# Optimization experiments

Measured on AMD Instinct MI355X. Metric: run time of the kernel, lower is better.

## Reference

```python
import jax, jax.numpy as jnp
import numpy as np

N, F, H, D = 50000, 128, 8, 16   # nodes, node features, heads, per-head dim (F == H*D -> Identity residual)
E, G = 800000, 512               # edges, graphs
HD = H * D


def _xavier(key, shape):
    fan = sum(shape[-2:]) if len(shape) >= 2 else shape[0] + 1
    lim = (6.0 / (shape[-2] + shape[-1])) ** 0.5 if len(shape) >= 2 else (6.0 / fan) ** 0.5
    return jax.random.uniform(key, shape, jnp.float32, -lim, lim)


def setup_inputs() -> dict:
    key = jax.random.key(0)
    ks = jax.random.split(key, 10)
    x = jax.random.normal(ks[0], (N, F), jnp.float32)
    edge_index = jax.random.randint(ks[1], (2, E), 0, N, dtype=jnp.int64)
    batch = jnp.sort(jax.random.randint(ks[2], (N,), 0, G, dtype=jnp.int64))
    W_src = _xavier(ks[3], (HD, F))
    W_dst = _xavier(ks[4], (HD, F))
    double_attn = _xavier(ks[5], (1, H, D))  # xavier over last two dims
    bias = jnp.zeros((HD,), jnp.float32)
    prelu_alpha = jnp.float32(0.25)          # nn.PReLU() default single weight
    w_weighting = _xavier(ks[6], (1, HD))
    b_weighting = jnp.zeros((1,), jnp.float32)
    w_score = _xavier(ks[7], (HD, HD))
    b_score = jnp.zeros((HD,), jnp.float32)
    return {
        "x": x, "edge_index": edge_index, "batch": batch,
        "W_src": W_src, "W_dst": W_dst, "double_attn": double_attn,
        "bias": bias, "prelu_alpha": prelu_alpha,
        "w_weighting": w_weighting, "b_weighting": b_weighting,
        "w_score": w_score, "b_score": b_score,
    }


def reference(x, edge_index, batch, W_src, W_dst, double_attn, bias, prelu_alpha,
              w_weighting, b_weighting, w_score, b_score):
    src, dst = edge_index[0], edge_index[1]
    # dropout is identity in eval mode
    src_p = (x @ W_src.T).reshape(N, H, D)    # [N,H,D]
    dst_p = (x @ W_dst.T).reshape(N, H, D)
    # edge-wise attention logits: gather + LeakyReLU(0.2) + dot with attention vector
    e = src_p[src] + dst_p[dst]               # [E,H,D]
    e = jnp.where(e > 0, e, 0.2 * e)
    logits = jnp.einsum('ehd,ohd->eh', e, double_attn)  # [E,H] (double_attn has leading 1)
    # segment softmax over destination nodes (global max shift, as in original)
    exp = jnp.exp(logits - logits.max())
    denom = jax.ops.segment_sum(exp, dst, num_segments=N)  # [N,H]
    alpha = exp / (denom[dst] + 1e-16)        # [E,H]
    # weighted aggregation of source projections
    msg = src_p[src] * alpha[:, :, None]      # [E,H,D]
    out = jax.ops.segment_sum(msg, dst, num_segments=N)    # [N,H,D]
    out = out + x.reshape(N, H, D)            # residual (Identity since F == H*D)
    out = out.reshape(N, HD) + bias           # concat heads + bias
    out = jnp.where(out > 0, out, prelu_alpha * out)       # PReLU activation
    # ReadoutPhase: gated sum pooling + max pooling per graph, concatenated
    weighted = jax.nn.sigmoid(out @ w_weighting.T + b_weighting)  # [N,1]
    score = out @ w_score.T + b_score                              # [N,HD]
    g_sum = jax.ops.segment_sum(weighted * score, batch, num_segments=G)  # [G,HD]
    g_max = jax.ops.segment_max(out, batch, num_segments=G)              # [G,HD]
    readout = jnp.concatenate([g_sum, g_max], axis=1)                     # [G,2*HD]
    return out, readout
```

## Files before the change

### kernel.cpp

```cpp
#include <hip/hip_runtime.h>

#define NODES 50000
#define FEAT 128
#define EDGES 800000
#define GRAPHS 512
#define NB 196
#define CHUNK 4096
#define ABLK 196
#define BCAP 8192
#define PROJ_BLOCKS 782

typedef unsigned int u32;
typedef unsigned short u16;
typedef __attribute__((ext_vector_type(8))) short short8;
typedef __attribute__((ext_vector_type(4))) float v4f;
typedef __attribute__((ext_vector_type(4))) u32 u32x4;
typedef __attribute__((ext_vector_type(2))) float f2;

static __device__ __forceinline__ float bflo(u32 u){ return __uint_as_float(u << 16); }
static __device__ __forceinline__ float bfhi(u32 u){ return __uint_as_float(u & 0xffff0000u); }
static __device__ __forceinline__ u16 f2bf(float f){
  u32 u = __float_as_uint(f);
  u32 r = u + 0x7fffu + ((u >> 16) & 1u);
  return (u16)(r >> 16);
}
static __device__ __forceinline__ u32 packbf(float a, float b){
  return (u32)f2bf(a) | ((u32)f2bf(b) << 16);
}
static __device__ __forceinline__ f2 unpk(u32 u){ f2 r; r.x = bflo(u); r.y = bfhi(u); return r; }
static __device__ __forceinline__ f2 vmax2(f2 a, f2 b){ f2 r; r.x = fmaxf(a.x,b.x); r.y = fmaxf(a.y,b.y); return r; }

#define LROW 68
__global__ __launch_bounds__(256) void proj_hist_kernel(
    const float* __restrict__ x, const float* __restrict__ Wsrc,
    const float* __restrict__ Wdst, u16* __restrict__ srcp, u16* __restrict__ dstp,
    const int* __restrict__ ei, int* __restrict__ bcount)
{
  __shared__ u32 x_lds[64 * LROW];
  __shared__ int cnt[NB];
  const int t = threadIdx.x;

  if (blockIdx.x >= PROJ_BLOCKS){
    const int b = blockIdx.x - PROJ_BLOCKS;
    for (int k = t; k < NB; k += 256) cnt[k] = 0;
    __syncthreads();
    const int e0 = b * CHUNK;
    const int e1 = (e0 + CHUNK < EDGES) ? e0 + CHUNK : EDGES;
    for (int e = e0 + t; e < e1; e += 256)
      atomicAdd(&cnt[ei[EDGES + e] >> 8], 1);
    __syncthreads();
    for (int k = t; k < NB; k += 256) bcount[b * NB + k] = cnt[k];
    return;
  }

  const int node0 = blockIdx.x * 64;
  const int rows_valid = NODES - node0 < 64 ? NODES - node0 : 64;
  const float4* xp = (const float4*)(x + (size_t)node0 * 128);
  for (int idx = t; idx < rows_valid * 32; idx += 256){
    const float4 v = xp[idx];
    const int row = idx >> 5, cq = idx & 31;
    x_lds[row * LROW + cq * 2]     = packbf(v.x, v.y);
    x_lds[row * LROW + cq * 2 + 1] = packbf(v.z, v.w);
  }

  const int wave = t >> 6, lane = t & 63;
  const int r16 = lane & 15;
  const int quad = lane >> 4;
  const int ko = quad * 4;
  const int n0 = wave * 32;

  short8 bs[2][4], bd[2][4];
  #pragma unroll
  for (int nt = 0; nt < 2; ++nt){
    const int col = n0 + nt * 16 + r16;
    #pragma unroll
    for (int k = 0; k < 4; ++k){
      const float4* wp = (const float4*)(Wsrc + col * 128 + quad * 8 + k * 32);
      float4 w0 = wp[0], w1 = wp[1];
      u32x4 pk; pk.x = packbf(w0.x,w0.y); pk.y = packbf(w0.z,w0.w);
      pk.z = packbf(w1.x,w1.y); pk.w = packbf(w1.z,w1.w);
      bs[nt][k] = __builtin_bit_cast(short8, pk);
      const float4* vp = (const float4*)(Wdst + col * 128 + quad * 8 + k * 32);
      float4 v0 = vp[0], v1 = vp[1];
      u32x4 qk; qk.x = packbf(v0.x,v0.y); qk.y = packbf(v0.z,v0.w);
      qk.z = packbf(v1.x,v1.y); qk.w = packbf(v1.z,v1.w);
      bd[nt][k] = __builtin_bit_cast(short8, qk);
    }
  }
  __syncthreads();

  #pragma unroll
  for (int mt = 0; mt < 4; ++mt){
    const int node_base = node0 + mt * 16;
    if (node_base >= NODES) break;
    short8 afr[4];
    #pragma unroll
    for (int k = 0; k < 4; ++k)
      afr[k] = *(const short8*)&x_lds[(mt * 16 + r16) * LROW + ko + k * 16];
    v4f s0 = {0.f,0.f,0.f,0.f}, s1 = s0, d0 = s0, d1 = s0;
    #pragma unroll
    for (int k = 0; k < 4; ++k){
      s0 = __builtin_amdgcn_mfma_f32_16x16x32_bf16(afr[k], bs[0][k], s0, 0, 0, 0);
      s1 = __builtin_amdgcn_mfma_f32_16x16x32_bf16(afr[k], bs[1][k], s1, 0, 0, 0);
      d0 = __builtin_amdgcn_mfma_f32_16x16x32_bf16(afr[k], bd[0][k], d0, 0, 0, 0);
      d1 = __builtin_amdgcn_mfma_f32_16x16x32_bf16(afr[k], bd[1][k], d1, 0, 0, 0);
    }
    const int node = node_base + quad * 4;
    u16* so0 = srcp + ((size_t)(wave*2)   * NODES + node) * 16 + r16;
    u16* so1 = srcp + ((size_t)(wave*2+1) * NODES + node) * 16 + r16;
    u16* dd0 = dstp + ((size_t)(wave*2)   * NODES + node) * 16 + r16;
    u16* dd1 = dstp + ((size_t)(wave*2+1) * NODES + node) * 16 + r16;
    #pragma unroll
    for (int r = 0; r < 4; ++r){
      so0[r * 16] = f2bf(s0[r]);
      so1[r * 16] = f2bf(s1[r]);
      dd0[r * 16] = f2bf(d0[r]);
      dd1[r * 16] = f2bf(d1[r]);
    }
  }
}

__global__ __launch_bounds__(256) void bucket_scatter_kernel(
    const int* __restrict__ ei, const int* __restrict__ bcount,
    int* __restrict__ bstart_g, u32* __restrict__ ebuf, float* __restrict__ wsum)
{
  __shared__ int tot[256];
  __shared__ int bstart_s[NB + 1];
  __shared__ int obase_s[NB];
  __shared__ int cur[NB];
  const int b = blockIdx.x, t = threadIdx.x;
  const int nid = b * 256 + t;
  if (nid < NODES) wsum[nid] = 0.f;
  int total = 0, obase = 0;
  if (t < NB){
    int run = 0;
    for (int q = 0; q < ABLK; ++q){
      if (q == b) obase = run;
      run += bcount[q * NB + t];
    }
    total = run;
  }
  tot[t] = total;
  __syncthreads();
  const int v = total;
  for (int off = 1; off < 256; off <<= 1){
    const int add = (t >= off) ? tot[t - off] : 0;
    __syncthreads();
    tot[t] += add;
    __syncthreads();
  }
  if (t < NB){
    bstart_s[t] = tot[t] - v;
    obase_s[t] = obase;
    cur[t] = 0;
  }
  if (t == NB - 1) bstart_s[NB] = tot[t];
  __syncthreads();
  if (b == 0 && t <= NB) bstart_g[t] = bstart_s[t];

  const int e0 = b * CHUNK;
  const int e1 = (e0 + CHUNK < EDGES) ? e0 + CHUNK : EDGES;
  for (int e = e0 + t; e < e1; e += 256){
    const int d = ei[EDGES + e];
    const int s = ei[e];
    const int k = d >> 8;
    const int r = atomicAdd(&cur[k], 1);
    ebuf[bstart_s[k] + obase_s[k] + r] = (u32)s | ((u32)(d & 255) << 16);
  }
}

__global__ __launch_bounds__(256) void bucket_csr_kernel(
    const u32* __restrict__ ebuf, const int* __restrict__ bstart,
    int* __restrict__ row_start, u16* __restrict__ srclist)
{
  __shared__ int cnt[256], excl[256], cur[256];
  __shared__ u32 loc[BCAP];
  const int k = blockIdx.x, t = threadIdx.x;
  const int base = bstart[k];
  int ne = bstart[k + 1] - base;
  if (ne > BCAP) ne = BCAP;
  cnt[t] = 0;
  __syncthreads();
  for (int j = t; j < ne; j += 256)
    atomicAdd(&cnt[(ebuf[base + j] >> 16) & 255], 1);
  __syncthreads();
  const int v = cnt[t];
  for (int off = 1; off < 256; off <<= 1){
    const int add = (t >= off) ? cnt[t - off] : 0;
    __syncthreads();
    cnt[t] += add;
    __syncthreads();
  }
  excl[t] = cnt[t] - v;
  cur[t] = cnt[t] - v;
  __syncthreads();
  const int node = k * 256 + t;
  if (node <= NODES) row_start[node] = base + excl[t];
  for (int j = t; j < ne; j += 256){
    const u32 e = ebuf[base + j];
    const int p = atomicAdd(&cur[(e >> 16) & 255], 1);
    loc[p] = e & 0xFFFFu;
  }
  __syncthreads();
  for (int j = t; j < ne; j += 256)
    srclist[base + j] = (u16)loc[j];
}

__global__ __launch_bounds__(256, 4) void aggregate_kernel(
    const u16* __restrict__ srcp, const u16* __restrict__ dstp,
    const int* __restrict__ row_start, const u16* __restrict__ srclist,
    const float* __restrict__ x, const float* __restrict__ attn,
    const float* __restrict__ bias, const float* __restrict__ palpha,
    const float* __restrict__ ww, float* __restrict__ outp,
    float* __restrict__ wsum)
{
  const int h   = blockIdx.x & 7;
  const int grp = blockIdx.x >> 3;
  const int wv = threadIdx.x >> 6;
  const int lane = threadIdx.x & 63;
  const int nd = lane >> 3;
  const int es = lane & 7;
  const int i = grp * 32 + wv * 8 + nd;
  const bool vn = i < NODES;
  const int ic = vn ? i : NODES - 1;
  const size_t hN = (size_t)h * NODES;
  const uint4* sp = (const uint4*)srcp;

  f2 d2[8], a2[8];
  {
    const uint4 dA = ((const uint4*)dstp)[(hN + ic) * 2];
    const uint4 dB = ((const uint4*)dstp)[(hN + ic) * 2 + 1];
    d2[0]=unpk(dA.x); d2[1]=unpk(dA.y); d2[2]=unpk(dA.z); d2[3]=unpk(dA.w);
    d2[4]=unpk(dB.x); d2[5]=unpk(dB.y); d2[6]=unpk(dB.z); d2[7]=unpk(dB.w);
    const float4* ap = (const float4*)(attn + h * 16);
    const float4 a0 = ap[0], a1 = ap[1], a2v = ap[2], a3v = ap[3];
    a2[0].x=a0.x;  a2[0].y=a0.y;  a2[1].x=a0.z;  a2[1].y=a0.w;
    a2[2].x=a1.x;  a2[2].y=a1.y;  a2[3].x=a1.z;  a2[3].y=a1.w;
    a2[4].x=a2v.x; a2[4].y=a2v.y; a2[5].x=a2v.z; a2[5].y=a2v.w;
    a2[6].x=a3v.x; a2[6].y=a3v.y; a2[7].x=a3v.z; a2[7].y=a3v.w;
  }
  const int lo = vn ? row_start[i] : 0;
  const int hi = vn ? row_start[i + 1] : 0;
  const int deg = hi - lo;
  const int nb = (deg + 7) >> 3;
  int nbw = nb;
  { int o = __shfl_xor(nbw, 8);  if (o > nbw) nbw = o; }
  { int o = __shfl_xor(nbw, 16); if (o > nbw) nbw = o; }
  { int o = __shfl_xor(nbw, 32); if (o > nbw) nbw = o; }

  f2 acc[8];
  #pragma unroll
  for (int q = 0; q < 8; ++q){ acc[q].x = 0.f; acc[q].y = 0.f; }
  float denom = 0.f;

  auto FETCH = [&](int c, uint4& A, uint4& B, bool& v){
    const int j = c * 8 + es;
    v = j < deg;
    const int s = v ? (int)srclist[lo + j] : 0;
    const uint4* rp = sp + (hN + s) * 2;
    A = rp[0]; B = rp[1];
  };
  auto COMP = [&](bool v, const uint4& A, const uint4& B){
    f2 sv[8];
    sv[0]=unpk(A.x); sv[1]=unpk(A.y); sv[2]=unpk(A.z); sv[3]=unpk(A.w);
    sv[4]=unpk(B.x); sv[5]=unpk(B.y); sv[6]=unpk(B.z); sv[7]=unpk(B.w);
    f2 p; p.x = 0.f; p.y = 0.f;
    #pragma unroll
    for (int q = 0; q < 8; ++q){
      f2 e = sv[q] + d2[q];
      e = vmax2(e, e * 0.2f);
      p += e * a2[q];
    }
    const float w = v ? __expf(p.x + p.y) : 0.f;
    denom += w;
    f2 w2; w2.x = w; w2.y = w;
    #pragma unroll
    for (int q = 0; q < 8; ++q) acc[q] += sv[q] * w2;
  };

  uint4 A0, B0, A1, B1; bool v0 = false, v1 = false;
  if (nbw > 0) FETCH(0, A0, B0, v0);
  if (nbw > 1) FETCH(1, A1, B1, v1);
  if (nbw > 0){ COMP(v0, A0, B0); if (nbw > 2) FETCH(2, A0, B0, v0); }
  if (nbw > 1){ COMP(v1, A1, B1); if (nbw > 3) FETCH(3, A1, B1, v1); }
  if (nbw > 2) COMP(v0, A0, B0);
  if (nbw > 3) COMP(v1, A1, B1);
  if (nbw > 4){
    for (int c = 4; c < nbw; ++c){
      uint4 TA, TB; bool tv;
      FETCH(c, TA, TB, tv);
      COMP(tv, TA, TB);
    }
  }

  denom += __shfl_xor(denom, 1);
  denom += __shfl_xor(denom, 2);
  denom += __shfl_xor(denom, 4);
  const float inv = 1.f / (denom + 1e-16f);

  float v8[8];
  #pragma unroll
  for (int q = 0; q < 4; ++q){
    const float gx = (es & 4) ? acc[q].x : acc[4 + q].x;
    const float gy = (es & 4) ? acc[q].y : acc[4 + q].y;
    const float rx = __shfl_xor(gx, 4);
    const float ry = __shfl_xor(gy, 4);
    v8[2*q]   = ((es & 4) ? acc[4 + q].x : acc[q].x) + rx;
    v8[2*q+1] = ((es & 4) ? acc[4 + q].y : acc[q].y) + ry;
  }
  float v4a[4];
  #pragma unroll
  for (int q = 0; q < 2; ++q){
    const float gx = (es & 2) ? v8[2*q]   : v8[4 + 2*q];
    const float gy = (es & 2) ? v8[2*q+1] : v8[4 + 2*q+1];
    const float rx = __shfl_xor(gx, 2);
    const float ry = __shfl_xor(gy, 2);
    v4a[2*q]   = ((es & 2) ? v8[4 + 2*q]   : v8[2*q]) + rx;
    v4a[2*q+1] = ((es & 2) ? v8[4 + 2*q+1] : v8[2*q+1]) + ry;
  }
  float r0, r1;
  {
    const float g0 = (es & 1) ? v4a[0] : v4a[2];
    const float g1 = (es & 1) ? v4a[1] : v4a[3];
    const float q0 = __shfl_xor(g0, 1);
    const float q1 = __shfl_xor(g1, 1);
    r0 = ((es & 1) ? v4a[2] : v4a[0]) + q0;
    r1 = ((es & 1) ? v4a[3] : v4a[1]) + q1;
  }

  const int col = h * 16 + es * 2;
  const f2 xr = *(const f2*)(x + (size_t)ic * 128 + col);
  const f2 bv = *(const f2*)(bias + col);
  const float al = palpha[0];
  const float t0 = fmaf(r0, inv, xr.x) + bv.x;
  const float t1 = fmaf(r1, inv, xr.y) + bv.y;
  const float o0 = (t0 > 0.f) ? t0 : al * t0;
  const float o1 = (t1 > 0.f) ? t1 : al * t1;
  if (vn){
    f2 ov; ov.x = o0; ov.y = o1;
    *(f2*)(outp + (size_t)i * 128 + col) = ov;
  }
  const f2 gv = *(const f2*)(ww + col);
  float z = o0 * gv.x + o1 * gv.y;
  z += __shfl_xor(z, 1);
  z += __shfl_xor(z, 2);
  z += __shfl_xor(z, 4);
  if (vn && es == 0) atomicAdd(&wsum[i], z);
}

__global__ __launch_bounds__(256) void readout_kernel(
    const float* __restrict__ outp, const float* __restrict__ wsumv,
    const int* __restrict__ batchv, const float* __restrict__ bw,
    const float* __restrict__ wscore, const float* __restrict__ bscore,
    float* __restrict__ ro)
{
  __shared__ int range_s[2];
  __shared__ float wsum_s[128];
  __shared__ float max_s[128];
  __shared__ float wtot_s[2];
  __shared__ float part_s[256];
  const int g = blockIdx.x, t = threadIdx.x;
  const int col = t & 127, grp = t >> 7;
  const float bw0 = bw[0];
  if (t < 2){
    const int target = g + t;
    int lo = 0, hi = NODES;
    while (lo < hi){ const int m = (lo + hi) >> 1; if (batchv[m] < target) lo = m + 1; else hi = m; }
    range_s[t] = lo;
  }
  __syncthreads();
  const int lo = range_s[0], hi = range_s[1];
  float acc = 0.f, vmax = -INFINITY, wacc = 0.f;
  for (int n = lo + grp; n < hi; n += 2){
    const float w = 1.f / (1.f + __expf(-(wsumv[n] + bw0)));
    const float v = outp[n * 128 + col];
    acc = fmaf(w, v, acc);
    vmax = fmaxf(vmax, v);
    if (col == 0) wacc += w;
  }
  part_s[t] = acc;
  if (col == 0) wtot_s[grp] = wacc;
  __syncthreads();
  if (grp == 0) wsum_s[col] = acc + part_s[col + 128];
  __syncthreads();
  part_s[t] = vmax;
  __syncthreads();
  if (grp == 0) max_s[col] = fmaxf(vmax, part_s[col + 128]);
  const float wtot = wtot_s[0] + wtot_s[1];
  __syncthreads();
  float dot = 0.f;
  const float* wr = wscore + col * 128 + grp * 64;
  const float* xs = wsum_s + grp * 64;
  #pragma unroll
  for (int k = 0; k < 64; ++k) dot = fmaf(wr[k], xs[k], dot);
  part_s[t] = dot;
  __syncthreads();
  if (grp == 0){
    const float s = dot + part_s[col + 128] + wtot * bscore[col];
    ro[g * 256 + col] = s;
    ro[g * 256 + 128 + col] = max_s[col];
  }
}

extern "C" void kernel_launch(void* const* d_in, const int* in_sizes, int n_in,
                              void* d_out, int out_size, void* d_ws, size_t ws_size,
                              hipStream_t stream)
{
  const float* x      = (const float*)d_in[0];
  const int*   ei     = (const int*)d_in[1];
  const int*   batchv = (const int*)d_in[2];
  const float* Wsrc   = (const float*)d_in[3];
  const float* Wdst   = (const float*)d_in[4];
  const float* attn   = (const float*)d_in[5];
  const float* bias   = (const float*)d_in[6];
  const float* palpha = (const float*)d_in[7];
  const float* ww     = (const float*)d_in[8];
  const float* bw     = (const float*)d_in[9];
  const float* wsc    = (const float*)d_in[10];
  const float* bsc    = (const float*)d_in[11];

  char* ws = (char*)d_ws;
  u16*  srcp      = (u16*) (ws + 0);
  u16*  dstp      = (u16*) (ws + 12800000);
  u16*  srclist   = (u16*) (ws + 25600000);
  int*  row_start = (int*) (ws + 28800000);
  int*  bcount    = (int*) (ws + 29000192);
  int*  bstart    = (int*) (ws + 29153856);
  float* wsum     = (float*)(ws + 29154688);

  float* outp = (float*)d_out;
  float* ro = outp + NODES * FEAT;
  u32* ebuf = (u32*)d_out;

  proj_hist_kernel<<<PROJ_BLOCKS + ABLK, 256, 0, stream>>>(
      x, Wsrc, Wdst, srcp, dstp, ei, bcount);
  bucket_scatter_kernel<<<ABLK, 256, 0, stream>>>(ei, bcount, bstart, ebuf, wsum);
  bucket_csr_kernel<<<NB, 256, 0, stream>>>(ebuf, bstart, row_start, srclist);
  const int ngrp = (NODES + 31) / 32;
  aggregate_kernel<<<ngrp * 8, 256, 0, stream>>>(srcp, dstp, row_start, srclist,
                                                 x, attn, bias, palpha, ww,
                                                 outp, wsum);
  readout_kernel<<<GRAPHS, 256, 0, stream>>>(outp, wsum, batchv, bw, wsc, bsc, ro);
}
```

Baseline: 223.9 us.

## Prepack bf16 weights in histogram kernel and deepen aggregate prefetch to four

Splits the fused projection/histogram kernel so that the histogram blocks also convert W_src/W_dst to packed bf16 once, and the projection kernel loads the prepacked weights instead of reconverting fp32 weights in every block. The aggregate kernel's software pipeline goes from two to four in-flight edge chunk fetches to hide more gather latency. This adds an extra kernel launch, loses the old overlap of histogram with projection, and increases register pressure in aggregate.

```diff
diff --git a/kernel.cpp b/kernel.cpp
--- a/kernel.cpp
+++ b/kernel.cpp
@@ -8,7 +8,6 @@
 #define CHUNK 4096
 #define ABLK 196
 #define BCAP 8192
-#define PROJ_BLOCKS 782
 
 typedef unsigned int u32;
 typedef unsigned short u16;
@@ -30,18 +29,15 @@
 static __device__ __forceinline__ f2 unpk(u32 u){ f2 r; r.x = bflo(u); r.y = bfhi(u); return r; }
 static __device__ __forceinline__ f2 vmax2(f2 a, f2 b){ f2 r; r.x = fmaxf(a.x,b.x); r.y = fmaxf(a.y,b.y); return r; }
 
-#define LROW 68
-__global__ __launch_bounds__(256) void proj_hist_kernel(
-    const float* __restrict__ x, const float* __restrict__ Wsrc,
-    const float* __restrict__ Wdst, u16* __restrict__ srcp, u16* __restrict__ dstp,
-    const int* __restrict__ ei, int* __restrict__ bcount)
-{
-  __shared__ u32 x_lds[64 * LROW];
+__global__ __launch_bounds__(256) void hist_pack_kernel(
+    const int* __restrict__ ei, int* __restrict__ bcount,
+    const float* __restrict__ Wsrc, const float* __restrict__ Wdst,
+    u32* __restrict__ wpk)
+{
   __shared__ int cnt[NB];
   const int t = threadIdx.x;
-
-  if (blockIdx.x >= PROJ_BLOCKS){
-    const int b = blockIdx.x - PROJ_BLOCKS;
+  if (blockIdx.x < ABLK){
+    const int b = blockIdx.x;
     for (int k = t; k < NB; k += 256) cnt[k] = 0;
     __syncthreads();
     const int e0 = b * CHUNK;
@@ -52,6 +48,20 @@
     for (int k = t; k < NB; k += 256) bcount[b * NB + k] = cnt[k];
     return;
   }
+  const int idx = (blockIdx.x - ABLK) * 256 + t;
+  const f2 a = *(const f2*)(Wsrc + 2 * idx);
+  const f2 b = *(const f2*)(Wdst + 2 * idx);
+  wpk[idx]         = packbf(a.x, a.y);
+  wpk[16384 + idx] = packbf(b.x, b.y);
+}
+
+#define LROW 68
+__global__ __launch_bounds__(256) void proj_kernel(
+    const float* __restrict__ x, const u32* __restrict__ wpk,
+    u16* __restrict__ srcp, u16* __restrict__ dstp)
+{
+  __shared__ u32 x_lds[64 * LROW];
+  const int t = threadIdx.x;
 
   const int node0 = blockIdx.x * 64;
   const int rows_valid = NODES - node0 < 64 ? NODES - node0 : 64;
@@ -70,21 +80,15 @@
   const int n0 = wave * 32;
 
   short8 bs[2][4], bd[2][4];
+  const u32* wps = wpk;
+  const u32* wpd = wpk + 16384;
   #pragma unroll
   for (int nt = 0; nt < 2; ++nt){
     const int col = n0 + nt * 16 + r16;
     #pragma unroll
     for (int k = 0; k < 4; ++k){
-      const float4* wp = (const float4*)(Wsrc + col * 128 + quad * 8 + k * 32);
-      float4 w0 = wp[0], w1 = wp[1];
-      u32x4 pk; pk.x = packbf(w0.x,w0.y); pk.y = packbf(w0.z,w0.w);
-      pk.z = packbf(w1.x,w1.y); pk.w = packbf(w1.z,w1.w);
-      bs[nt][k] = __builtin_bit_cast(short8, pk);
-      const float4* vp = (const float4*)(Wdst + col * 128 + quad * 8 + k * 32);
-      float4 v0 = vp[0], v1 = vp[1];
-      u32x4 qk; qk.x = packbf(v0.x,v0.y); qk.y = packbf(v0.z,v0.w);
-      qk.z = packbf(v1.x,v1.y); qk.w = packbf(v1.z,v1.w);
-      bd[nt][k] = __builtin_bit_cast(short8, qk);
+      bs[nt][k] = *(const short8*)(wps + col * 64 + quad * 4 + k * 16);
+      bd[nt][k] = *(const short8*)(wpd + col * 64 + quad * 4 + k * 16);
     }
   }
   __syncthreads();
@@ -278,15 +282,22 @@
     for (int q = 0; q < 8; ++q) acc[q] += sv[q] * w2;
   };
 
-  uint4 A0, B0, A1, B1; bool v0 = false, v1 = false;
+  uint4 A0,B0,A1,B1,A2,B2,A3,B3;
+  bool v0=false, v1=false, v2=false, v3=false;
   if (nbw > 0) FETCH(0, A0, B0, v0);
   if (nbw > 1) FETCH(1, A1, B1, v1);
-  if (nbw > 0){ COMP(v0, A0, B0); if (nbw > 2) FETCH(2, A0, B0, v0); }
-  if (nbw > 1){ COMP(v1, A1, B1); if (nbw > 3) FETCH(3, A1, B1, v1); }
-  if (nbw > 2) COMP(v0, A0, B0);
-  if (nbw > 3) COMP(v1, A1, B1);
-  if (nbw > 4){
-    for (int c = 4; c < nbw; ++c){
+  if (nbw > 2) FETCH(2, A2, B2, v2);
+  if (nbw > 3) FETCH(3, A3, B3, v3);
+  if (nbw > 0){ COMP(v0, A0, B0); if (nbw > 4) FETCH(4, A0, B0, v0); }
+  if (nbw > 1){ COMP(v1, A1, B1); if (nbw > 5) FETCH(5, A1, B1, v1); }
+  if (nbw > 2){ COMP(v2, A2, B2); if (nbw > 6) FETCH(6, A2, B2, v2); }
+  if (nbw > 3){ COMP(v3, A3, B3); if (nbw > 7) FETCH(7, A3, B3, v3); }
+  if (nbw > 4) COMP(v0, A0, B0);
+  if (nbw > 5) COMP(v1, A1, B1);
+  if (nbw > 6) COMP(v2, A2, B2);
+  if (nbw > 7) COMP(v3, A3, B3);
+  if (nbw > 8){
+    for (int c = 8; c < nbw; ++c){
       uint4 TA, TB; bool tv;
       FETCH(c, TA, TB, tv);
       COMP(tv, TA, TB);
@@ -431,9 +442,10 @@
   float* outp = (float*)d_out;
   float* ro = outp + NODES * FEAT;
   u32* ebuf = (u32*)d_out;
-
-  proj_hist_kernel<<<PROJ_BLOCKS + ABLK, 256, 0, stream>>>(
-      x, Wsrc, Wdst, srcp, dstp, ei, bcount);
+  u32* wpk = (u32*)((char*)d_out + 8388608);
+
+  hist_pack_kernel<<<ABLK + 64, 256, 0, stream>>>(ei, bcount, Wsrc, Wdst, wpk);
+  proj_kernel<<<782, 256, 0, stream>>>(x, wpk, srcp, dstp);
   bucket_scatter_kernel<<<ABLK, 256, 0, stream>>>(ei, bcount, bstart, ebuf, wsum);
   bucket_csr_kernel<<<NB, 256, 0, stream>>>(ebuf, bstart, row_start, srclist);
   const int ngrp = (NODES + 31) / 32;
```

Result: slower. 236.0 us (+5.4%).
